# Kernel tuning notes

Measured on AMD Instinct MI355X. Metric: run time of the kernel, lower is better.

## Reference

```python
import jax, jax.numpy as jnp
import numpy as np

INPUT_DIM = 1024
HIDDEN_DIM = 1024


def setup_inputs() -> dict:
    key = jax.random.key(0)
    ks = jax.random.split(key, 7)
    B, S = 4, 2048
    s = 1.0 / np.sqrt(INPUT_DIM)
    x = jax.random.normal(ks[0], (B, S, INPUT_DIM), dtype=jnp.float32)
    Wq = jax.random.normal(ks[1], (HIDDEN_DIM, INPUT_DIM), dtype=jnp.float32) * s
    bq = jnp.zeros((HIDDEN_DIM,), dtype=jnp.float32)
    Wk = jax.random.normal(ks[2], (HIDDEN_DIM, INPUT_DIM), dtype=jnp.float32) * s
    bk = jnp.zeros((HIDDEN_DIM,), dtype=jnp.float32)
    Wv = jax.random.normal(ks[3], (HIDDEN_DIM, INPUT_DIM), dtype=jnp.float32) * s
    bv = jnp.zeros((HIDDEN_DIM,), dtype=jnp.float32)
    return {"x": x, "Wq": Wq, "bq": bq, "Wk": Wk, "bk": bk, "Wv": Wv, "bv": bv}


def reference(x, Wq, bq, Wk, bk, Wv, bv):
    # Linear layers: y = x @ W.T + b (torch nn.Linear convention)
    q = jnp.einsum('bsi,hi->bsh', x, Wq) + bq
    k = jnp.einsum('bsi,hi->bsh', x, Wk) + bk
    v = jnp.einsum('bsi,hi->bsh', x, Wv) + bv
    scale = 1.0 / jnp.sqrt(jnp.asarray(q.shape[-1], dtype=q.dtype))
    scores = jnp.einsum('bsh,bth->bst', q, k) * scale  # [B,S,S]
    attention_weights = jax.nn.softmax(scores, axis=-1)
    weighted_sum = jnp.einsum('bst,bth->bsh', attention_weights, v)
    return (weighted_sum, attention_weights)
```

## Files before the change

kernel.cpp:

```cpp
#include <hip/hip_runtime.h>
#include <hip/hip_bf16.h>
#include <cstdint>


typedef __bf16 bf16x8 __attribute__((ext_vector_type(8)));
typedef float  f32x4  __attribute__((ext_vector_type(4)));

__device__ __forceinline__ void load_lds16(const __bf16* g, __bf16* l) {
    __builtin_amdgcn_global_load_lds(
        (const __attribute__((address_space(1))) void*)g,
        (__attribute__((address_space(3))) void*)l,
        16, 0, 0);
}

__global__ __launch_bounds__(256) void cvt_f32_bf16(
        const float* __restrict__ src, __bf16* __restrict__ dst, int n8) {
    int i = blockIdx.x * blockDim.x + threadIdx.x;
    if (i >= n8) return;
    const float4* s4 = (const float4*)src;
    float4 a = s4[2 * i], b = s4[2 * i + 1];
    bf16x8 o;
    o[0] = (__bf16)a.x; o[1] = (__bf16)a.y; o[2] = (__bf16)a.z; o[3] = (__bf16)a.w;
    o[4] = (__bf16)b.x; o[5] = (__bf16)b.y; o[6] = (__bf16)b.z; o[7] = (__bf16)b.w;
    ((bf16x8*)dst)[i] = o;
}

__global__ __launch_bounds__(256) void pack_bias3(
        const float* __restrict__ a, const float* __restrict__ b,
        const float* __restrict__ c, float* __restrict__ o) {
    int i = blockIdx.x * blockDim.x + threadIdx.x;
    if (i < 1024) { o[i] = a[i]; o[i + 1024] = b[i]; o[i + 2048] = c[i]; }
}

template <int MODE>
__global__ __launch_bounds__(256, 3) void gemm_nt(
        const __bf16* __restrict__ A, const __bf16* __restrict__ Bt,
        void* __restrict__ C0, void* __restrict__ C1, void* __restrict__ C2,
        const float* __restrict__ bias,
        int lda, int ldb, int ldc, long sA, long sB, long sC,
        int K, float scale) {
    __shared__ __bf16 lA[128 * 64];
    __shared__ __bf16 lB[128 * 64];

    const int tid  = threadIdx.x;
    const int lane = tid & 63;
    const int wave = tid >> 6;
    const int mblk = blockIdx.y * 128;
    const int nblk = blockIdx.x * 128;
    const int z    = blockIdx.z;
    A  += (long)z * sA;
    Bt += (long)z * sB;

    const int wm = (wave >> 1) * 64;
    const int wn = (wave & 1) * 64;

    f32x4 zero = {0.f, 0.f, 0.f, 0.f};
    f32x4 acc[4][4];
#pragma unroll
    for (int i = 0; i < 4; ++i)
#pragma unroll
        for (int j = 0; j < 4; ++j) acc[i][j] = zero;

    const int rsel = lane & 15;
    const int quad = lane >> 4;

    int srow[4], scol[4];
#pragma unroll
    for (int it = 0; it < 4; ++it) {
        int s  = tid + it * 256;
        srow[it] = s >> 3;
        scol[it] = ((s & 7) ^ (srow[it] & 7)) * 8;
    }

    for (int k0 = 0; k0 < K; k0 += 64) {
#pragma unroll
        for (int it = 0; it < 4; ++it) {
            int s = tid + it * 256;
            load_lds16(A  + (long)(mblk + srow[it]) * lda + k0 + scol[it], lA + s * 8);
            load_lds16(Bt + (long)(nblk + srow[it]) * ldb + k0 + scol[it], lB + s * 8);
        }
        __syncthreads();

#pragma unroll
        for (int half = 0; half < 2; ++half) {
            const int cq = quad + half * 4;
            bf16x8 fa[4], fb[4];
#pragma unroll
            for (int i = 0; i < 4; ++i) {
                int ra = wm + i * 16 + rsel;
                fa[i] = *(const bf16x8*)&lA[(ra * 8 + (cq ^ (ra & 7))) * 8];
                int rb = wn + i * 16 + rsel;
                fb[i] = *(const bf16x8*)&lB[(rb * 8 + (cq ^ (rb & 7))) * 8];
            }
#pragma unroll
            for (int i = 0; i < 4; ++i)
#pragma unroll
                for (int j = 0; j < 4; ++j)
                    acc[i][j] = __builtin_amdgcn_mfma_f32_16x16x32_bf16(
                        fa[i], fb[j], acc[i][j], 0, 0, 0);
        }
        __syncthreads();
    }

    const int rq = quad * 4;
#pragma unroll
    for (int i = 0; i < 4; ++i) {
#pragma unroll
        for (int j = 0; j < 4; ++j) {
            const int n = nblk + wn + j * 16 + rsel;
            if constexpr (MODE == 0) {
                __bf16* C = (n < 1024) ? (__bf16*)C0
                          : (n < 2048) ? (__bf16*)C1 : (__bf16*)C2;
                const int col = n & 1023;
                float bv = bias[n];
#pragma unroll
                for (int r = 0; r < 4; ++r) {
                    int m = mblk + wm + i * 16 + rq + r;
                    C[(long)m * ldc + col] = (__bf16)(acc[i][j][r] + bv);
                }
            } else if constexpr (MODE == 1) {
                float* C = (float*)C0 + (long)z * sC;
#pragma unroll
                for (int r = 0; r < 4; ++r) {
                    int m = mblk + wm + i * 16 + rq + r;
                    C[(long)m * ldc + n] = acc[i][j][r] * scale;
                }
            } else {
                float* C = (float*)C0 + (long)z * sC;
#pragma unroll
                for (int r = 0; r < 4; ++r) {
                    int m = mblk + wm + i * 16 + rq + r;
                    C[(long)m * ldc + n] = acc[i][j][r];
                }
            }
        }
    }
}

__global__ __launch_bounds__(256) void softmax_rows(
        float* __restrict__ P, __bf16* __restrict__ Pb) {
    const long row = blockIdx.x;
    float*  p  = P  + row * 2048;
    __bf16* pb = Pb + row * 2048;
    const int tid  = threadIdx.x;
    const int lane = tid & 63;
    const int wave = tid >> 6;

    float4 v0 = ((const float4*)p)[tid * 2];
    float4 v1 = ((const float4*)p)[tid * 2 + 1];
    float e[8] = {v0.x, v0.y, v0.z, v0.w, v1.x, v1.y, v1.z, v1.w};

    float mx = e[0];
#pragma unroll
    for (int i = 1; i < 8; ++i) mx = fmaxf(mx, e[i]);
#pragma unroll
    for (int o = 1; o < 64; o <<= 1) mx = fmaxf(mx, __shfl_xor(mx, o, 64));

    __shared__ float redm[4], reds[4];
    if (lane == 0) redm[wave] = mx;
    __syncthreads();
    mx = fmaxf(fmaxf(redm[0], redm[1]), fmaxf(redm[2], redm[3]));

    float sum = 0.f;
#pragma unroll
    for (int i = 0; i < 8; ++i) { e[i] = __expf(e[i] - mx); sum += e[i]; }
#pragma unroll
    for (int o = 1; o < 64; o <<= 1) sum += __shfl_xor(sum, o, 64);
    if (lane == 0) reds[wave] = sum;
    __syncthreads();
    sum = reds[0] + reds[1] + reds[2] + reds[3];
    const float inv = 1.f / sum;

    float4 o0, o1;
    o0.x = e[0] * inv; o0.y = e[1] * inv; o0.z = e[2] * inv; o0.w = e[3] * inv;
    o1.x = e[4] * inv; o1.y = e[5] * inv; o1.z = e[6] * inv; o1.w = e[7] * inv;
    ((float4*)p)[tid * 2]     = o0;
    ((float4*)p)[tid * 2 + 1] = o1;
    bf16x8 ob;
    ob[0] = (__bf16)o0.x; ob[1] = (__bf16)o0.y; ob[2] = (__bf16)o0.z; ob[3] = (__bf16)o0.w;
    ob[4] = (__bf16)o1.x; ob[5] = (__bf16)o1.y; ob[6] = (__bf16)o1.z; ob[7] = (__bf16)o1.w;
    ((bf16x8*)pb)[tid] = ob;
}

__global__ __launch_bounds__(256) void transpose_v(
        const __bf16* __restrict__ src, __bf16* __restrict__ dst) {
    __shared__ __bf16 t[32][33];
    const int tx = threadIdx.x, ty = threadIdx.y;
    const int tileC = blockIdx.x * 32;
    const int tileR = blockIdx.y * 32;
    const long zs = (long)blockIdx.z * 2048 * 1024;
    const long zd = (long)blockIdx.z * 1024 * 2048;
#pragma unroll
    for (int k = 0; k < 4; ++k) {
        int r = ty * 4 + k;
        t[r][tx] = src[zs + (long)(tileR + r) * 1024 + tileC + tx];
    }
    __syncthreads();
#pragma unroll
    for (int k = 0; k < 4; ++k) {
        int c = ty * 4 + k;
        dst[zd + (long)(tileC + c) * 2048 + tileR + tx] = t[tx][c];
    }
}

extern "C" void kernel_launch(void* const* d_in, const int* in_sizes, int n_in,
                              void* d_out, int out_size, void* d_ws, size_t ws_size,
                              hipStream_t stream) {
    const float* x  = (const float*)d_in[0];
    const float* Wq = (const float*)d_in[1];
    const float* bq = (const float*)d_in[2];
    const float* Wk = (const float*)d_in[3];
    const float* bk = (const float*)d_in[4];
    const float* Wv = (const float*)d_in[5];
    const float* bv = (const float*)d_in[6];

    const int  S = 2048, H = 1024, I = 1024, B = 4;
    const long MS = (long)B * S;
    float* out_ws  = (float*)d_out;
    float* out_att = (float*)d_out + (long)B * S * H;

    char* w = (char*)d_ws;
    __bf16* x_bf   = (__bf16*)w; w += MS * I * 2;
    __bf16* wqkv   = (__bf16*)w; w += (long)3 * H * I * 2;
    float*  bias3  = (float*)w;  w += 4096 * 4;
    __bf16* q_bf   = (__bf16*)w; w += MS * H * 2;
    __bf16* k_bf   = (__bf16*)w; w += MS * H * 2;
    __bf16* v_bf   = (__bf16*)w; w += MS * H * 2;
    __bf16* vt_bf  = (__bf16*)w; w += MS * H * 2;
    __bf16* p_bf   = (__bf16*)w; w += (long)B * S * S * 2;

    {
        int n8 = (int)(MS * I / 8);
        cvt_f32_bf16<<<dim3((n8 + 255) / 256), dim3(256), 0, stream>>>(x, x_bf, n8);
        int w8 = H * I / 8;
        cvt_f32_bf16<<<dim3((w8 + 255) / 256), dim3(256), 0, stream>>>(Wq, wqkv, w8);
        cvt_f32_bf16<<<dim3((w8 + 255) / 256), dim3(256), 0, stream>>>(Wk, wqkv + (long)H * I, w8);
        cvt_f32_bf16<<<dim3((w8 + 255) / 256), dim3(256), 0, stream>>>(Wv, wqkv + (long)2 * H * I, w8);
        pack_bias3<<<dim3(4), dim3(256), 0, stream>>>(bq, bk, bv, bias3);
    }

    gemm_nt<0><<<dim3(24, 64, 1), dim3(256), 0, stream>>>(
        x_bf, wqkv, q_bf, k_bf, v_bf, bias3,
        1024, 1024, 1024, 0, 0, 0, 1024, 1.f);

    transpose_v<<<dim3(32, 64, 4), dim3(32, 8), 0, stream>>>(v_bf, vt_bf);

    gemm_nt<1><<<dim3(16, 16, 4), dim3(256), 0, stream>>>(
        q_bf, k_bf, out_att, nullptr, nullptr, nullptr,
        1024, 1024, 2048, (long)S * H, (long)S * H, (long)S * S, 1024, 0.03125f);

    softmax_rows<<<dim3(8192), dim3(256), 0, stream>>>(out_att, p_bf);

    gemm_nt<2><<<dim3(8, 16, 4), dim3(256), 0, stream>>>(
        p_bf, vt_bf, out_ws, nullptr, nullptr, nullptr,
        2048, 2048, 1024, (long)S * S, (long)S * H, (long)S * H, 2048, 1.f);
}
```

Measured before the change: 318.1 us.

## Switch GEMM to 32x32x16 MFMA and merge conversion kernels into one launch

The GEMM inner loop now issues 32x32x16 bf16 MFMAs on 2x2 tiles per wave instead of 16x16x32 MFMAs on 4x4 tiles. This halves the LDS fragment reads per k-step and may raise MFMA throughput, but the epilogue now stores 16 strided rows per lane. Separately, the four f32-to-bf16 conversion launches and the bias pack are merged into one kernel to cut launch overhead.

```diff
diff --git a/kernel.cpp b/kernel.cpp
--- a/kernel.cpp
+++ b/kernel.cpp
@@ -3,8 +3,8 @@
 #include <cstdint>
 
 
-typedef __bf16 bf16x8 __attribute__((ext_vector_type(8)));
-typedef float  f32x4  __attribute__((ext_vector_type(4)));
+typedef __bf16 bf16x8  __attribute__((ext_vector_type(8)));
+typedef float  f32x16  __attribute__((ext_vector_type(16)));
 
 __device__ __forceinline__ void load_lds16(const __bf16* g, __bf16* l) {
     __builtin_amdgcn_global_load_lds(
@@ -13,23 +13,40 @@
         16, 0, 0);
 }
 
-__global__ __launch_bounds__(256) void cvt_f32_bf16(
-        const float* __restrict__ src, __bf16* __restrict__ dst, int n8) {
-    int i = blockIdx.x * blockDim.x + threadIdx.x;
-    if (i >= n8) return;
+__global__ __launch_bounds__(256) void cvt_all(
+        const float* __restrict__ x,
+        const float* __restrict__ wq, const float* __restrict__ wk,
+        const float* __restrict__ wv,
+        const float* __restrict__ bq, const float* __restrict__ bk,
+        const float* __restrict__ bv,
+        __bf16* __restrict__ xb, __bf16* __restrict__ wb,
+        float* __restrict__ bias3) {
+    const long NX = 1048576, NW = 131072;
+    long i = (long)blockIdx.x * 256 + threadIdx.x;
+    const float* src; __bf16* dst; long c;
+    if (i < NX) { src = x; dst = xb; c = i; }
+    else if (i < NX + 3 * NW) {
+        long j = i - NX;
+        src = (j < NW) ? wq : (j < 2 * NW) ? wk : wv;
+        c = j % NW;
+        dst = wb + (j / NW) * (NW * 8);
+    } else if (i < NX + 3 * NW + 384) {
+        long cidx = i - (NX + 3 * NW);
+        int seg = (int)(cidx >> 7);
+        const float* bs = (seg == 0) ? bq : (seg == 1) ? bk : bv;
+        long off = (cidx & 127) * 8;
+        float4 a = *(const float4*)(bs + off);
+        float4 b = *(const float4*)(bs + off + 4);
+        *(float4*)(bias3 + cidx * 8)     = a;
+        *(float4*)(bias3 + cidx * 8 + 4) = b;
+        return;
+    } else return;
     const float4* s4 = (const float4*)src;
-    float4 a = s4[2 * i], b = s4[2 * i + 1];
+    float4 a = s4[2 * c], b = s4[2 * c + 1];
     bf16x8 o;
     o[0] = (__bf16)a.x; o[1] = (__bf16)a.y; o[2] = (__bf16)a.z; o[3] = (__bf16)a.w;
     o[4] = (__bf16)b.x; o[5] = (__bf16)b.y; o[6] = (__bf16)b.z; o[7] = (__bf16)b.w;
-    ((bf16x8*)dst)[i] = o;
-}
-
-__global__ __launch_bounds__(256) void pack_bias3(
-        const float* __restrict__ a, const float* __restrict__ b,
-        const float* __restrict__ c, float* __restrict__ o) {
-    int i = blockIdx.x * blockDim.x + threadIdx.x;
-    if (i < 1024) { o[i] = a[i]; o[i + 1024] = b[i]; o[i + 2048] = c[i]; }
+    ((bf16x8*)dst)[c] = o;
 }
 
 template <int MODE>
@@ -54,15 +71,16 @@
     const int wm = (wave >> 1) * 64;
     const int wn = (wave & 1) * 64;
 
-    f32x4 zero = {0.f, 0.f, 0.f, 0.f};
-    f32x4 acc[4][4];
-#pragma unroll
-    for (int i = 0; i < 4; ++i)
-#pragma unroll
-        for (int j = 0; j < 4; ++j) acc[i][j] = zero;
-
-    const int rsel = lane & 15;
-    const int quad = lane >> 4;
+    f32x16 acc[2][2];
+#pragma unroll
+    for (int i = 0; i < 2; ++i)
+#pragma unroll
+        for (int j = 0; j < 2; ++j)
+#pragma unroll
+            for (int r = 0; r < 16; ++r) acc[i][j][r] = 0.f;
+
+    const int rowsel = lane & 31;
+    const int khalf  = lane >> 5;
 
     int srow[4], scol[4];
 #pragma unroll
@@ -82,54 +100,53 @@
         __syncthreads();
 
 #pragma unroll
-        for (int half = 0; half < 2; ++half) {
-            const int cq = quad + half * 4;
-            bf16x8 fa[4], fb[4];
-#pragma unroll
-            for (int i = 0; i < 4; ++i) {
-                int ra = wm + i * 16 + rsel;
-                fa[i] = *(const bf16x8*)&lA[(ra * 8 + (cq ^ (ra & 7))) * 8];
-                int rb = wn + i * 16 + rsel;
-                fb[i] = *(const bf16x8*)&lB[(rb * 8 + (cq ^ (rb & 7))) * 8];
+        for (int kk = 0; kk < 4; ++kk) {
+            const int cq = kk * 2 + khalf;
+            bf16x8 fa[2], fb[2];
+#pragma unroll
+            for (int t = 0; t < 2; ++t) {
+                int ra = wm + t * 32 + rowsel;
+                fa[t] = *(const bf16x8*)&lA[(ra * 8 + (cq ^ (ra & 7))) * 8];
+                int rb = wn + t * 32 + rowsel;
+                fb[t] = *(const bf16x8*)&lB[(rb * 8 + (cq ^ (rb & 7))) * 8];
             }
 #pragma unroll
-            for (int i = 0; i < 4; ++i)
-#pragma unroll
-                for (int j = 0; j < 4; ++j)
-                    acc[i][j] = __builtin_amdgcn_mfma_f32_16x16x32_bf16(
+            for (int i = 0; i < 2; ++i)
+#pragma unroll
+                for (int j = 0; j < 2; ++j)
+                    acc[i][j] = __builtin_amdgcn_mfma_f32_32x32x16_bf16(
                         fa[i], fb[j], acc[i][j], 0, 0, 0);
         }
         __syncthreads();
     }
 
-    const int rq = quad * 4;
-#pragma unroll
-    for (int i = 0; i < 4; ++i) {
-#pragma unroll
-        for (int j = 0; j < 4; ++j) {
-            const int n = nblk + wn + j * 16 + rsel;
+#pragma unroll
+    for (int i = 0; i < 2; ++i) {
+#pragma unroll
+        for (int j = 0; j < 2; ++j) {
+            const int n = nblk + wn + j * 32 + rowsel;
             if constexpr (MODE == 0) {
                 __bf16* C = (n < 1024) ? (__bf16*)C0
                           : (n < 2048) ? (__bf16*)C1 : (__bf16*)C2;
                 const int col = n & 1023;
                 float bv = bias[n];
 #pragma unroll
-                for (int r = 0; r < 4; ++r) {
-                    int m = mblk + wm + i * 16 + rq + r;
+                for (int r = 0; r < 16; ++r) {
+                    int m = mblk + wm + i * 32 + (r & 3) + 8 * (r >> 2) + 4 * khalf;
                     C[(long)m * ldc + col] = (__bf16)(acc[i][j][r] + bv);
                 }
             } else if constexpr (MODE == 1) {
                 float* C = (float*)C0 + (long)z * sC;
 #pragma unroll
-                for (int r = 0; r < 4; ++r) {
-                    int m = mblk + wm + i * 16 + rq + r;
+                for (int r = 0; r < 16; ++r) {
+                    int m = mblk + wm + i * 32 + (r & 3) + 8 * (r >> 2) + 4 * khalf;
                     C[(long)m * ldc + n] = acc[i][j][r] * scale;
                 }
             } else {
                 float* C = (float*)C0 + (long)z * sC;
 #pragma unroll
-                for (int r = 0; r < 4; ++r) {
-                    int m = mblk + wm + i * 16 + rq + r;
+                for (int r = 0; r < 16; ++r) {
+                    int m = mblk + wm + i * 32 + (r & 3) + 8 * (r >> 2) + 4 * khalf;
                     C[(long)m * ldc + n] = acc[i][j][r];
                 }
             }
@@ -230,13 +247,9 @@
     __bf16* p_bf   = (__bf16*)w; w += (long)B * S * S * 2;
 
     {
-        int n8 = (int)(MS * I / 8);
-        cvt_f32_bf16<<<dim3((n8 + 255) / 256), dim3(256), 0, stream>>>(x, x_bf, n8);
-        int w8 = H * I / 8;
-        cvt_f32_bf16<<<dim3((w8 + 255) / 256), dim3(256), 0, stream>>>(Wq, wqkv, w8);
-        cvt_f32_bf16<<<dim3((w8 + 255) / 256), dim3(256), 0, stream>>>(Wk, wqkv + (long)H * I, w8);
-        cvt_f32_bf16<<<dim3((w8 + 255) / 256), dim3(256), 0, stream>>>(Wv, wqkv + (long)2 * H * I, w8);
-        pack_bias3<<<dim3(4), dim3(256), 0, stream>>>(bq, bk, bv, bias3);
+        long tot = 1048576 + 3 * 131072 + 384;
+        cvt_all<<<dim3((unsigned)((tot + 255) / 256)), dim3(256), 0, stream>>>(
+            x, Wq, Wk, Wv, bq, bk, bv, x_bf, wqkv, bias3);
     }
 
     gemm_nt<0><<<dim3(24, 64, 1), dim3(256), 0, stream>>>(
```

After: 321.5 us. About the same (+1.1%).
